# Optimization experiments

Hardware: AMD Instinct MI355X
Metric: run time of the kernel (lower is better)

## Reference

```python
import jax, jax.numpy as jnp
import numpy as np

N = 50000
IN_FEAT = 128
HIDDEN = 128
NUM_CLASS = 64
E = 1600000


def setup_inputs() -> dict:
    key = jax.random.key(0)
    ks = jax.random.split(key, 10)
    s = 1.0 / np.sqrt(HIDDEN)
    return {
        "x": jax.random.normal(ks[0], (N, IN_FEAT), dtype=jnp.float32),
        "edge_index": jax.random.randint(ks[1], (2, E), 0, N, dtype=jnp.int64),
        "We": jax.random.uniform(ks[2], (IN_FEAT, HIDDEN), jnp.float32, -s, s),
        "be": jax.random.uniform(ks[3], (HIDDEN,), jnp.float32, -s, s),
        "W1": jax.random.uniform(ks[4], (HIDDEN, HIDDEN), jnp.float32, -s, s),
        "b1": jax.random.uniform(ks[5], (HIDDEN,), jnp.float32, -s, s),
        "W2": jax.random.uniform(ks[6], (HIDDEN, HIDDEN), jnp.float32, -s, s),
        "b2": jax.random.uniform(ks[7], (HIDDEN,), jnp.float32, -s, s),
        "Wo": jax.random.uniform(ks[8], (HIDDEN, NUM_CLASS), jnp.float32, -s, s),
        "bo": jax.random.uniform(ks[9], (NUM_CLASS,), jnp.float32, -s, s),
    }


def _gcn_conv(h, src, dst, norm, W, b, n):
    # h: [N, H]; src/dst/norm: [E+N] (self-loops appended); GCNConv math:
    # out = scatter_add(norm * (h @ W)[src] -> dst) + b
    h = h @ W
    msg = h[src] * norm[:, None]  # gather + scale  [E+N, H]
    out = jax.ops.segment_sum(msg, dst, num_segments=n)
    return out + b


def reference(x, edge_index, We, be, W1, b1, W2, b2, Wo, bo):
    n = x.shape[0]
    loops = jnp.arange(n, dtype=edge_index.dtype)
    src = jnp.concatenate([edge_index[0], loops])
    dst = jnp.concatenate([edge_index[1], loops])
    # symmetric normalization D^{-1/2} (A+I) D^{-1/2}
    deg = jax.ops.segment_sum(jnp.ones_like(dst, dtype=x.dtype), dst, num_segments=n)
    dinv = jnp.where(deg > 0, jax.lax.rsqrt(deg), 0.0)
    norm = dinv[src] * dinv[dst]

    h = x @ We + be                       # encoder
    h = jax.nn.relu(_gcn_conv(h, src, dst, norm, W1, b1, n))
    h = jax.nn.relu(_gcn_conv(h, src, dst, norm, W2, b2, n))
    return h @ Wo + bo                    # decoder
```

## Files before the change

kernel.cpp:

```cpp
#include <hip/hip_runtime.h>
#include <hip/hip_fp16.h>


#define WS_ALIGN(x) (((x) + 255) & ~(size_t)255)
#define RS 100
#define BCHUNK 8192

typedef _Float16 f16x8 __attribute__((ext_vector_type(8)));
typedef float f32x4 __attribute__((ext_vector_type(4)));

__global__ void detect_i64_kernel(const unsigned* __restrict__ p, int* __restrict__ flag) {
    __shared__ int any;
    if (threadIdx.x == 0) any = 0;
    __syncthreads();
    int nz = 0;
    for (int i = threadIdx.x; i < 2048; i += blockDim.x)
        nz |= (p[2 * i + 1] != 0u) ? 1 : 0;
    if (nz) atomicOr(&any, 1);
    __syncthreads();
    if (threadIdx.x == 0) *flag = (any == 0) ? 1 : 0;
}

__global__ void zero_u32_kernel(unsigned* __restrict__ a, int n) {
    int i = blockIdx.x * blockDim.x + threadIdx.x;
    if (i < n) a[i] = 0u;
}

__global__ __launch_bounds__(256) void bucket_kernel(
    const void* __restrict__ ep, const int* __restrict__ flag,
    unsigned* __restrict__ bkt, unsigned* __restrict__ bfill_pad,
    int E, int nbuck, int capB) {
    __shared__ unsigned lcnt[512];
    __shared__ unsigned gcur[512];
    const int tid = threadIdx.x;
    for (int i = tid; i < nbuck; i += 256) lcnt[i] = 0;
    __syncthreads();
    const int base = blockIdx.x * BCHUNK;
    const int end = min(base + BCHUNK, E);
    const int i64 = *flag;
    if (i64) {
        const long long* p = (const long long*)ep;
        for (int i = base + tid; i < end; i += 256) {
            int d = (int)p[(size_t)E + i];
            atomicAdd(&lcnt[d / RS], 1u);
        }
    } else {
        const int* p = (const int*)ep;
        for (int i = base + tid; i < end; i += 256) {
            int d = p[(size_t)E + i];
            atomicAdd(&lcnt[d / RS], 1u);
        }
    }
    __syncthreads();
    for (int i = tid; i < nbuck; i += 256)
        gcur[i] = atomicAdd(&bfill_pad[i << 4], lcnt[i]);
    __syncthreads();
    if (i64) {
        const long long* p = (const long long*)ep;
        for (int i = base + tid; i < end; i += 256) {
            int s = (int)p[i];
            int d = (int)p[(size_t)E + i];
            int part = d / RS;
            int ld = d - part * RS;
            unsigned pos = atomicAdd(&gcur[part], 1u);
            if (pos < (unsigned)capB)
                bkt[(size_t)part * capB + pos] = ((unsigned)ld << 24) | (unsigned)s;
        }
    } else {
        const int* p = (const int*)ep;
        for (int i = base + tid; i < end; i += 256) {
            int s = p[i];
            int d = p[(size_t)E + i];
            int part = d / RS;
            int ld = d - part * RS;
            unsigned pos = atomicAdd(&gcur[part], 1u);
            if (pos < (unsigned)capB)
                bkt[(size_t)part * capB + pos] = ((unsigned)ld << 24) | (unsigned)s;
        }
    }
}

__global__ __launch_bounds__(512) void bucket_scan_kernel(
    const unsigned* __restrict__ bfill_pad, unsigned* __restrict__ ebase,
    int* __restrict__ rowp, int nbuck, int capB, int n) {
    __shared__ unsigned lds[512];
    const int tid = threadIdx.x;
    unsigned v = 0;
    if (tid < nbuck) {
        v = bfill_pad[tid << 4];
        if (v > (unsigned)capB) v = capB;
    }
    lds[tid] = v;
    __syncthreads();
    for (int off = 1; off < 512; off <<= 1) {
        unsigned add = (tid >= off) ? lds[tid - off] : 0;
        __syncthreads();
        lds[tid] += add;
        __syncthreads();
    }
    if (tid < nbuck) ebase[tid] = lds[tid] - v;
    if (tid == 511) rowp[n] = (int)lds[511];
}

__global__ __launch_bounds__(256) void csr_from_bucket_kernel(
    const unsigned* __restrict__ bkt, const unsigned* __restrict__ bfill_pad,
    const unsigned* __restrict__ ebase,
    int* __restrict__ rowp, float* __restrict__ dinv, int* __restrict__ col,
    int capB, int n) {
    __shared__ unsigned hist[RS];
    __shared__ int fillo[RS];
    const int p = blockIdx.x;
    const int tid = threadIdx.x;
    for (int i = tid; i < RS; i += 256) hist[i] = 0;
    __syncthreads();
    unsigned cnt = bfill_pad[p << 4];
    if (cnt > (unsigned)capB) cnt = capB;
    const unsigned* bp = bkt + (size_t)p * capB;
    for (unsigned e = tid; e < cnt; e += 256)
        atomicAdd(&hist[bp[e] >> 24], 1u);
    __syncthreads();
    if (tid == 0) {
        int run = (int)ebase[p];
        for (int i = 0; i < RS; ++i) { fillo[i] = run; run += (int)hist[i]; }
    }
    __syncthreads();
    const int lo = p * RS;
    for (int i = tid; i < RS; i += 256) {
        int node = lo + i;
        if (node < n) {
            rowp[node] = fillo[i];
            dinv[node] = rsqrtf((float)(hist[i] + 1u));
        }
    }
    for (unsigned e = tid; e < cnt; e += 256) {
        unsigned u = bp[e];
        int ld = (int)(u >> 24);
        int pos = atomicAdd(&fillo[ld], 1);
        col[pos] = (int)(u & 0xFFFFFFu);
    }
}

__global__ __launch_bounds__(256) void agg_pull_kernel(
    const int* __restrict__ rowp, const int* __restrict__ col,
    const float* __restrict__ dinv, const __half* __restrict__ t,
    const float* __restrict__ bias, __half* __restrict__ out, int n) {
    int node = blockIdx.x * 8 + (threadIdx.x >> 5);
    int lane = threadIdx.x & 31;
    if (node >= n) return;
    const uint2* T = (const uint2*)t;
    int j0 = rowp[node], j1 = rowp[node + 1];
    float dn = dinv[node];

    uint2 sraw = T[(size_t)node * 32 + lane];
    float2 s01 = __half22float2(*(const __half2*)&sraw.x);
    float2 s23 = __half22float2(*(const __half2*)&sraw.y);
    float4 acc = make_float4(s01.x, s01.y, s23.x, s23.y);

    int j = j0;
    for (; j + 7 < j1; j += 8) {
        int c[8];
        uint2 r[8];
#pragma unroll
        for (int k = 0; k < 8; ++k) c[k] = __builtin_nontemporal_load(col + j + k);
#pragma unroll
        for (int k = 0; k < 8; ++k) r[k] = T[(size_t)c[k] * 32 + lane];
#pragma unroll
        for (int k = 0; k < 8; ++k) {
            float2 f01 = __half22float2(*(const __half2*)&r[k].x);
            float2 f23 = __half22float2(*(const __half2*)&r[k].y);
            acc.x += f01.x; acc.y += f01.y; acc.z += f23.x; acc.w += f23.y;
        }
    }
    for (; j + 3 < j1; j += 4) {
        int c[4];
        uint2 r[4];
#pragma unroll
        for (int k = 0; k < 4; ++k) c[k] = __builtin_nontemporal_load(col + j + k);
#pragma unroll
        for (int k = 0; k < 4; ++k) r[k] = T[(size_t)c[k] * 32 + lane];
#pragma unroll
        for (int k = 0; k < 4; ++k) {
            float2 f01 = __half22float2(*(const __half2*)&r[k].x);
            float2 f23 = __half22float2(*(const __half2*)&r[k].y);
            acc.x += f01.x; acc.y += f01.y; acc.z += f23.x; acc.w += f23.y;
        }
    }
    for (; j < j1; ++j) {
        int c = __builtin_nontemporal_load(col + j);
        uint2 raw = T[(size_t)c * 32 + lane];
        float2 f01 = __half22float2(*(const __half2*)&raw.x);
        float2 f23 = __half22float2(*(const __half2*)&raw.y);
        acc.x += f01.x; acc.y += f01.y; acc.z += f23.x; acc.w += f23.y;
    }

    float4 b = ((const float4*)bias)[lane];
    float ox = fmaxf(fmaf(acc.x, dn, b.x), 0.f);
    float oy = fmaxf(fmaf(acc.y, dn, b.y), 0.f);
    float oz = fmaxf(fmaf(acc.z, dn, b.z), 0.f);
    float ow = fmaxf(fmaf(acc.w, dn, b.w), 0.f);
    __half2 h01 = __floats2half2_rn(ox, oy);
    __half2 h23 = __floats2half2_rn(oz, ow);
    uint2 packed;
    packed.x = *(unsigned*)&h01;
    packed.y = *(unsigned*)&h23;
    ((uint2*)(out + (size_t)node * 128))[lane] = packed;
}

__global__ void f32_to_f16_kernel(const float* __restrict__ in, __half* __restrict__ out, int n8) {
    int i = blockIdx.x * blockDim.x + threadIdx.x;
    if (i >= n8) return;
    const float4* in4 = (const float4*)in;
    float4 v0 = in4[2 * i], v1 = in4[2 * i + 1];
    __half2 h0 = __floats2half2_rn(v0.x, v0.y);
    __half2 h1 = __floats2half2_rn(v0.z, v0.w);
    __half2 h2 = __floats2half2_rn(v1.x, v1.y);
    __half2 h3 = __floats2half2_rn(v1.z, v1.w);
    uint4 p;
    p.x = *(unsigned*)&h0; p.y = *(unsigned*)&h1;
    p.z = *(unsigned*)&h2; p.w = *(unsigned*)&h3;
    *(uint4*)(out + (size_t)i * 8) = p;
}

__global__ void wfrag_kernel(const float* __restrict__ W, __half* __restrict__ Wf, int ncol) {
    int t = blockIdx.x * blockDim.x + threadIdx.x;
    int total = (ncol >> 4) * 4 * 64;
    if (t >= total) return;
    int lane = t & 63;
    int ks = (t >> 6) & 3;
    int c0 = t >> 8;
    int colw = c0 * 16 + (lane & 15);
    int k0 = ks * 32 + ((lane >> 4) << 3);
    __half vals[8];
#pragma unroll
    for (int j = 0; j < 8; ++j) vals[j] = __float2half(W[(size_t)(k0 + j) * ncol + colw]);
    *(uint4*)(Wf + (size_t)t * 8) = *(uint4*)vals;
}

__global__ __launch_bounds__(256) void gemm_mfma_kernel(
    const __half* __restrict__ A, const __half* __restrict__ Wf,
    const float* __restrict__ bias, const float* __restrict__ rowscale,
    void* __restrict__ C, int n, int ncol, int c_fp32) {
    const int wave = threadIdx.x >> 6;
    const int lane = threadIdx.x & 63;
    const int row0 = blockIdx.x * 64 + wave * 16;
    int ar = row0 + (lane & 15);
    if (ar >= n) ar = n - 1;
    const __half* abase = A + (size_t)ar * 128 + ((lane >> 4) << 3);
    f16x8 a0 = *(const f16x8*)(abase);
    f16x8 a1 = *(const f16x8*)(abase + 32);
    f16x8 a2 = *(const f16x8*)(abase + 64);
    f16x8 a3 = *(const f16x8*)(abase + 96);
    const int ncc = ncol >> 4;
    const int cic = lane & 15;
    const int rbase = (lane >> 4) << 2;
    float rs[4];
#pragma unroll
    for (int r = 0; r < 4; ++r) {
        int row = row0 + rbase + r;
        rs[r] = (rowscale && row < n) ? rowscale[row] : 1.f;
    }
    for (int c0 = 0; c0 < ncc; ++c0) {
        const f16x8* wf = (const f16x8*)Wf + (size_t)c0 * 256 + lane;
        f32x4 acc = {0.f, 0.f, 0.f, 0.f};
        acc = __builtin_amdgcn_mfma_f32_16x16x32_f16(a0, wf[0],   acc, 0, 0, 0);
        acc = __builtin_amdgcn_mfma_f32_16x16x32_f16(a1, wf[64],  acc, 0, 0, 0);
        acc = __builtin_amdgcn_mfma_f32_16x16x32_f16(a2, wf[128], acc, 0, 0, 0);
        acc = __builtin_amdgcn_mfma_f32_16x16x32_f16(a3, wf[192], acc, 0, 0, 0);
        int colc = (c0 << 4) + cic;
        float bv = bias ? bias[colc] : 0.f;
#pragma unroll
        for (int r = 0; r < 4; ++r) {
            int row = row0 + rbase + r;
            if (row < n) {
                float v = acc[r] * rs[r] + bv;
                if (c_fp32) ((float*)C)[(size_t)row * ncol + colc] = v;
                else        ((__half*)C)[(size_t)row * ncol + colc] = __float2half(v);
            }
        }
    }
}

extern "C" void kernel_launch(void* const* d_in, const int* in_sizes, int n_in,
                              void* d_out, int out_size, void* d_ws, size_t ws_size,
                              hipStream_t stream) {
    const float* x  = (const float*)d_in[0];
    const void*  ei = d_in[1];
    const float* We = (const float*)d_in[2];
    const float* be = (const float*)d_in[3];
    const float* W1 = (const float*)d_in[4];
    const float* b1 = (const float*)d_in[5];
    const float* W2 = (const float*)d_in[6];
    const float* b2 = (const float*)d_in[7];
    const float* Wo = (const float*)d_in[8];
    const float* bo = (const float*)d_in[9];
    const int N = in_sizes[0] / 128;
    const int E = in_sizes[1] / 2;
    const int NC = in_sizes[9];
    const int nbuck = (N + RS - 1) / RS;
    const int capB = (E + nbuck - 1) / nbuck + 512;

    char* ws = (char*)d_ws;
    size_t off = 0;
    int*      flag = (int*)(ws + off);      off += 256;
    unsigned* bfil = (unsigned*)(ws + off); off += WS_ALIGN((size_t)nbuck * 64);
    unsigned* ebas = (unsigned*)(ws + off); off += WS_ALIGN((size_t)nbuck * 4);
    unsigned* bkt  = (unsigned*)(ws + off); off += WS_ALIGN((size_t)nbuck * capB * 4);
    float*    dinv = (float*)(ws + off);    off += WS_ALIGN((size_t)N * 4);
    int*      rowp = (int*)(ws + off);      off += WS_ALIGN((size_t)(N + 1) * 4);
    int*      colw = (int*)(ws + off);      off += WS_ALIGN((size_t)E * 4);
    __half*   WeF  = (__half*)(ws + off);   off += WS_ALIGN((size_t)128 * 128 * 2);
    __half*   W1F  = (__half*)(ws + off);   off += WS_ALIGN((size_t)128 * 128 * 2);
    __half*   W2F  = (__half*)(ws + off);   off += WS_ALIGN((size_t)128 * 128 * 2);
    __half*   WoF  = (__half*)(ws + off);   off += WS_ALIGN((size_t)128 * 64 * 2);
    __half*   xH   = (__half*)(ws + off);   off += WS_ALIGN((size_t)N * 128 * 2);
    __half*   hA   = (__half*)(ws + off);   off += WS_ALIGN((size_t)N * 128 * 2);
    __half*   tH   = (__half*)(ws + off);   off += WS_ALIGN((size_t)N * 128 * 2);

    const int nb_bucket = (E + BCHUNK - 1) / BCHUNK;
    const int nb_zero = (nbuck * 16 + 255) / 256;
    dim3 blk(256);

    detect_i64_kernel<<<1, 256, 0, stream>>>((const unsigned*)ei, flag);
    zero_u32_kernel<<<nb_zero, blk, 0, stream>>>(bfil, nbuck * 16);
    bucket_kernel<<<nb_bucket, blk, 0, stream>>>(ei, flag, bkt, bfil, E, nbuck, capB);
    bucket_scan_kernel<<<1, 512, 0, stream>>>(bfil, ebas, rowp, nbuck, capB, N);
    csr_from_bucket_kernel<<<nbuck, blk, 0, stream>>>(bkt, bfil, ebas, rowp, dinv, colw, capB, N);

    wfrag_kernel<<<8, 256, 0, stream>>>(We, WeF, 128);
    wfrag_kernel<<<8, 256, 0, stream>>>(W1, W1F, 128);
    wfrag_kernel<<<8, 256, 0, stream>>>(W2, W2F, 128);
    wfrag_kernel<<<4, 256, 0, stream>>>(Wo, WoF, NC);
    f32_to_f16_kernel<<<(N * 16 + 255) / 256, 256, 0, stream>>>(x, xH, N * 16);

    const int gemm_blocks = (N + 63) / 64;
    const int agg_blocks = (N + 7) / 8;

    gemm_mfma_kernel<<<gemm_blocks, blk, 0, stream>>>(xH, WeF, be, nullptr, hA, N, 128, 0);
    gemm_mfma_kernel<<<gemm_blocks, blk, 0, stream>>>(hA, W1F, nullptr, dinv, tH, N, 128, 0);
    agg_pull_kernel<<<agg_blocks, blk, 0, stream>>>(rowp, colw, dinv, tH, b1, hA, N);
    gemm_mfma_kernel<<<gemm_blocks, blk, 0, stream>>>(hA, W2F, nullptr, dinv, tH, N, 128, 0);
    agg_pull_kernel<<<agg_blocks, blk, 0, stream>>>(rowp, colw, dinv, tH, b2, hA, N);
    gemm_mfma_kernel<<<gemm_blocks, blk, 0, stream>>>(hA, WoF, bo, nullptr, d_out, N, NC, 1);
}
```

Baseline: 238.1 us.

## Fold encoder into first GCN weight and read fp32 input directly in GEMM

Precomputes We@W1 and be@W1 on device so the encoder GEMM and first conv GEMM become one GEMM that reads fp32 x directly, removing the x-to-fp16 conversion pass and one full N×128 intermediate round trip. The GEMM epilogue now applies bias before the row scale, so the folded bias is scaled correctly. Also merges the zeroing kernel into the detect kernel, the three weight-fragment kernels into one launch, and switches column loads from nontemporal to normal loads. It adds a small naive 128×128 matmul kernel, and rounding now happens on the combined weights rather than on the intermediate activations.

```diff
diff --git a/kernel.cpp b/kernel.cpp
--- a/kernel.cpp
+++ b/kernel.cpp
@@ -9,7 +9,8 @@
 typedef _Float16 f16x8 __attribute__((ext_vector_type(8)));
 typedef float f32x4 __attribute__((ext_vector_type(4)));
 
-__global__ void detect_i64_kernel(const unsigned* __restrict__ p, int* __restrict__ flag) {
+__global__ void detect_zero_kernel(const unsigned* __restrict__ p, int* __restrict__ flag,
+                                   unsigned* __restrict__ bfil, int nzero) {
     __shared__ int any;
     if (threadIdx.x == 0) any = 0;
     __syncthreads();
@@ -17,13 +18,9 @@
     for (int i = threadIdx.x; i < 2048; i += blockDim.x)
         nz |= (p[2 * i + 1] != 0u) ? 1 : 0;
     if (nz) atomicOr(&any, 1);
+    for (int i = threadIdx.x; i < nzero; i += blockDim.x) bfil[i] = 0u;
     __syncthreads();
     if (threadIdx.x == 0) *flag = (any == 0) ? 1 : 0;
-}
-
-__global__ void zero_u32_kernel(unsigned* __restrict__ a, int n) {
-    int i = blockIdx.x * blockDim.x + threadIdx.x;
-    if (i < n) a[i] = 0u;
 }
 
 __global__ __launch_bounds__(256) void bucket_kernel(
@@ -132,12 +129,52 @@
             dinv[node] = rsqrtf((float)(hist[i] + 1u));
         }
     }
+    __syncthreads();
     for (unsigned e = tid; e < cnt; e += 256) {
         unsigned u = bp[e];
         int ld = (int)(u >> 24);
         int pos = atomicAdd(&fillo[ld], 1);
         col[pos] = (int)(u & 0xFFFFFFu);
     }
+}
+
+__global__ __launch_bounds__(256) void wcomb_kernel(
+    const float* __restrict__ We, const float* __restrict__ W1,
+    const float* __restrict__ be, float* __restrict__ Wcomb,
+    float* __restrict__ bcomb) {
+    int t = blockIdx.x * 256 + threadIdx.x;
+    int r = t >> 7, c = t & 127;
+    float s = 0.f;
+    for (int k = 0; k < 128; ++k) s = fmaf(We[r * 128 + k], W1[k * 128 + c], s);
+    Wcomb[t] = s;
+    if (t < 128) {
+        float b = 0.f;
+        for (int k = 0; k < 128; ++k) b = fmaf(be[k], W1[k * 128 + t], b);
+        bcomb[t] = b;
+    }
+}
+
+__global__ __launch_bounds__(256) void wfrag3_kernel(
+    const float* __restrict__ Wa, __half* __restrict__ WaF,
+    const float* __restrict__ Wb, __half* __restrict__ WbF,
+    const float* __restrict__ Wc, __half* __restrict__ WcF, int nco) {
+    const float* W;
+    __half* Wf;
+    int ncol, t;
+    if (blockIdx.x < 8)       { W = Wa; Wf = WaF; ncol = 128; t = blockIdx.x * 256 + threadIdx.x; }
+    else if (blockIdx.x < 16) { W = Wb; Wf = WbF; ncol = 128; t = (blockIdx.x - 8) * 256 + threadIdx.x; }
+    else                      { W = Wc; Wf = WcF; ncol = nco; t = (blockIdx.x - 16) * 256 + threadIdx.x; }
+    int total = (ncol >> 4) * 4 * 64;
+    if (t >= total) return;
+    int lane = t & 63;
+    int ks = (t >> 6) & 3;
+    int c0 = t >> 8;
+    int colw = c0 * 16 + (lane & 15);
+    int k0 = ks * 32 + ((lane >> 4) << 3);
+    __half vals[8];
+#pragma unroll
+    for (int j = 0; j < 8; ++j) vals[j] = __float2half(W[(size_t)(k0 + j) * ncol + colw]);
+    *(uint4*)(Wf + (size_t)t * 8) = *(uint4*)vals;
 }
 
 __global__ __launch_bounds__(256) void agg_pull_kernel(
@@ -161,7 +198,7 @@
         int c[8];
         uint2 r[8];
 #pragma unroll
-        for (int k = 0; k < 8; ++k) c[k] = __builtin_nontemporal_load(col + j + k);
+        for (int k = 0; k < 8; ++k) c[k] = col[j + k];
 #pragma unroll
         for (int k = 0; k < 8; ++k) r[k] = T[(size_t)c[k] * 32 + lane];
 #pragma unroll
@@ -175,7 +212,7 @@
         int c[4];
         uint2 r[4];
 #pragma unroll
-        for (int k = 0; k < 4; ++k) c[k] = __builtin_nontemporal_load(col + j + k);
+        for (int k = 0; k < 4; ++k) c[k] = col[j + k];
 #pragma unroll
         for (int k = 0; k < 4; ++k) r[k] = T[(size_t)c[k] * 32 + lane];
 #pragma unroll
@@ -186,7 +223,7 @@
         }
     }
     for (; j < j1; ++j) {
-        int c = __builtin_nontemporal_load(col + j);
+        int c = col[j];
         uint2 raw = T[(size_t)c * 32 + lane];
         float2 f01 = __half22float2(*(const __half2*)&raw.x);
         float2 f23 = __half22float2(*(const __half2*)&raw.y);
@@ -206,50 +243,39 @@
     ((uint2*)(out + (size_t)node * 128))[lane] = packed;
 }
 
-__global__ void f32_to_f16_kernel(const float* __restrict__ in, __half* __restrict__ out, int n8) {
-    int i = blockIdx.x * blockDim.x + threadIdx.x;
-    if (i >= n8) return;
-    const float4* in4 = (const float4*)in;
-    float4 v0 = in4[2 * i], v1 = in4[2 * i + 1];
-    __half2 h0 = __floats2half2_rn(v0.x, v0.y);
-    __half2 h1 = __floats2half2_rn(v0.z, v0.w);
-    __half2 h2 = __floats2half2_rn(v1.x, v1.y);
-    __half2 h3 = __floats2half2_rn(v1.z, v1.w);
-    uint4 p;
-    p.x = *(unsigned*)&h0; p.y = *(unsigned*)&h1;
-    p.z = *(unsigned*)&h2; p.w = *(unsigned*)&h3;
-    *(uint4*)(out + (size_t)i * 8) = p;
-}
-
-__global__ void wfrag_kernel(const float* __restrict__ W, __half* __restrict__ Wf, int ncol) {
-    int t = blockIdx.x * blockDim.x + threadIdx.x;
-    int total = (ncol >> 4) * 4 * 64;
-    if (t >= total) return;
-    int lane = t & 63;
-    int ks = (t >> 6) & 3;
-    int c0 = t >> 8;
-    int colw = c0 * 16 + (lane & 15);
-    int k0 = ks * 32 + ((lane >> 4) << 3);
-    __half vals[8];
-#pragma unroll
-    for (int j = 0; j < 8; ++j) vals[j] = __float2half(W[(size_t)(k0 + j) * ncol + colw]);
-    *(uint4*)(Wf + (size_t)t * 8) = *(uint4*)vals;
+__device__ __forceinline__ f16x8 frag_from_f32(const float* p) {
+    float4 u = *(const float4*)p;
+    float4 v = *(const float4*)(p + 4);
+    f16x8 r;
+    r[0] = (_Float16)u.x; r[1] = (_Float16)u.y; r[2] = (_Float16)u.z; r[3] = (_Float16)u.w;
+    r[4] = (_Float16)v.x; r[5] = (_Float16)v.y; r[6] = (_Float16)v.z; r[7] = (_Float16)v.w;
+    return r;
 }
 
 __global__ __launch_bounds__(256) void gemm_mfma_kernel(
-    const __half* __restrict__ A, const __half* __restrict__ Wf,
+    const void* __restrict__ A, const __half* __restrict__ Wf,
     const float* __restrict__ bias, const float* __restrict__ rowscale,
-    void* __restrict__ C, int n, int ncol, int c_fp32) {
+    void* __restrict__ C, int n, int ncol, int a_fp32, int c_fp32) {
     const int wave = threadIdx.x >> 6;
     const int lane = threadIdx.x & 63;
     const int row0 = blockIdx.x * 64 + wave * 16;
     int ar = row0 + (lane & 15);
     if (ar >= n) ar = n - 1;
-    const __half* abase = A + (size_t)ar * 128 + ((lane >> 4) << 3);
-    f16x8 a0 = *(const f16x8*)(abase);
-    f16x8 a1 = *(const f16x8*)(abase + 32);
-    f16x8 a2 = *(const f16x8*)(abase + 64);
-    f16x8 a3 = *(const f16x8*)(abase + 96);
+    const int koff = (lane >> 4) << 3;
+    f16x8 a0, a1, a2, a3;
+    if (a_fp32) {
+        const float* ab = (const float*)A + (size_t)ar * 128 + koff;
+        a0 = frag_from_f32(ab);
+        a1 = frag_from_f32(ab + 32);
+        a2 = frag_from_f32(ab + 64);
+        a3 = frag_from_f32(ab + 96);
+    } else {
+        const __half* ab = (const __half*)A + (size_t)ar * 128 + koff;
+        a0 = *(const f16x8*)(ab);
+        a1 = *(const f16x8*)(ab + 32);
+        a2 = *(const f16x8*)(ab + 64);
+        a3 = *(const f16x8*)(ab + 96);
+    }
     const int ncc = ncol >> 4;
     const int cic = lane & 15;
     const int rbase = (lane >> 4) << 2;
@@ -272,7 +298,7 @@
         for (int r = 0; r < 4; ++r) {
             int row = row0 + rbase + r;
             if (row < n) {
-                float v = acc[r] * rs[r] + bv;
+                float v = (acc[r] + bv) * rs[r];
                 if (c_fp32) ((float*)C)[(size_t)row * ncol + colc] = v;
                 else        ((__half*)C)[(size_t)row * ncol + colc] = __float2half(v);
             }
@@ -308,37 +334,31 @@
     float*    dinv = (float*)(ws + off);    off += WS_ALIGN((size_t)N * 4);
     int*      rowp = (int*)(ws + off);      off += WS_ALIGN((size_t)(N + 1) * 4);
     int*      colw = (int*)(ws + off);      off += WS_ALIGN((size_t)E * 4);
-    __half*   WeF  = (__half*)(ws + off);   off += WS_ALIGN((size_t)128 * 128 * 2);
-    __half*   W1F  = (__half*)(ws + off);   off += WS_ALIGN((size_t)128 * 128 * 2);
+    float*    Wcmb = (float*)(ws + off);    off += WS_ALIGN((size_t)128 * 128 * 4);
+    float*    bcmb = (float*)(ws + off);    off += WS_ALIGN((size_t)128 * 4);
+    __half*   WcF  = (__half*)(ws + off);   off += WS_ALIGN((size_t)128 * 128 * 2);
     __half*   W2F  = (__half*)(ws + off);   off += WS_ALIGN((size_t)128 * 128 * 2);
     __half*   WoF  = (__half*)(ws + off);   off += WS_ALIGN((size_t)128 * 64 * 2);
-    __half*   xH   = (__half*)(ws + off);   off += WS_ALIGN((size_t)N * 128 * 2);
     __half*   hA   = (__half*)(ws + off);   off += WS_ALIGN((size_t)N * 128 * 2);
     __half*   tH   = (__half*)(ws + off);   off += WS_ALIGN((size_t)N * 128 * 2);
 
     const int nb_bucket = (E + BCHUNK - 1) / BCHUNK;
-    const int nb_zero = (nbuck * 16 + 255) / 256;
     dim3 blk(256);
 
-    detect_i64_kernel<<<1, 256, 0, stream>>>((const unsigned*)ei, flag);
-    zero_u32_kernel<<<nb_zero, blk, 0, stream>>>(bfil, nbuck * 16);
+    detect_zero_kernel<<<1, 256, 0, stream>>>((const unsigned*)ei, flag, bfil, nbuck * 16);
     bucket_kernel<<<nb_bucket, blk, 0, stream>>>(ei, flag, bkt, bfil, E, nbuck, capB);
     bucket_scan_kernel<<<1, 512, 0, stream>>>(bfil, ebas, rowp, nbuck, capB, N);
     csr_from_bucket_kernel<<<nbuck, blk, 0, stream>>>(bkt, bfil, ebas, rowp, dinv, colw, capB, N);
 
-    wfrag_kernel<<<8, 256, 0, stream>>>(We, WeF, 128);
-    wfrag_kernel<<<8, 256, 0, stream>>>(W1, W1F, 128);
-    wfrag_kernel<<<8, 256, 0, stream>>>(W2, W2F, 128);
-    wfrag_kernel<<<4, 256, 0, stream>>>(Wo, WoF, NC);
-    f32_to_f16_kernel<<<(N * 16 + 255) / 256, 256, 0, stream>>>(x, xH, N * 16);
+    wcomb_kernel<<<64, blk, 0, stream>>>(We, W1, be, Wcmb, bcmb);
+    wfrag3_kernel<<<20, blk, 0, stream>>>(Wcmb, WcF, W2, W2F, Wo, WoF, NC);
 
     const int gemm_blocks = (N + 63) / 64;
     const int agg_blocks = (N + 7) / 8;
 
-    gemm_mfma_kernel<<<gemm_blocks, blk, 0, stream>>>(xH, WeF, be, nullptr, hA, N, 128, 0);
-    gemm_mfma_kernel<<<gemm_blocks, blk, 0, stream>>>(hA, W1F, nullptr, dinv, tH, N, 128, 0);
+    gemm_mfma_kernel<<<gemm_blocks, blk, 0, stream>>>(x, WcF, bcmb, dinv, tH, N, 128, 1, 0);
     agg_pull_kernel<<<agg_blocks, blk, 0, stream>>>(rowp, colw, dinv, tH, b1, hA, N);
-    gemm_mfma_kernel<<<gemm_blocks, blk, 0, stream>>>(hA, W2F, nullptr, dinv, tH, N, 128, 0);
+    gemm_mfma_kernel<<<gemm_blocks, blk, 0, stream>>>(hA, W2F, nullptr, dinv, tH, N, 128, 0, 0);
     agg_pull_kernel<<<agg_blocks, blk, 0, stream>>>(rowp, colw, dinv, tH, b2, hA, N);
-    gemm_mfma_kernel<<<gemm_blocks, blk, 0, stream>>>(hA, WoF, bo, nullptr, d_out, N, NC, 1);
-}
+    gemm_mfma_kernel<<<gemm_blocks, blk, 0, stream>>>(hA, WoF, bo, nullptr, d_out, N, NC, 0, 1);
+}
```

Measured after the change: 212.8 us, median of 2. -10.6%, faster.
